# Optimization experiments

Hardware: AMD Instinct MI355X
Metric: run time of the kernel (lower is better)

Reference implementation:

```python
import jax, jax.numpy as jnp
import numpy as np

G, NP, F = 128, 1024, 16   # graphs, nodes per graph, node feature dim
K = 16                      # kNN neighbors (includes self, as in PyG knn)
H, L, OUT = 64, 64, 128     # edge-MLP hidden, latent, final output dims


def setup_inputs() -> dict:
    key = jax.random.key(0)
    ks = jax.random.split(key, 5)
    def w(i, shape, fan):
        return jax.random.normal(ks[i], shape, jnp.float32) / np.sqrt(fan)
    return {
        "x": jax.random.normal(ks[0], (G * NP, F), jnp.float32),
        "batch": jnp.repeat(jnp.arange(G, dtype=jnp.int32), NP),  # equal-size graphs
        "W1": w(1, (2 * F, H), 2 * F), "b1": jnp.zeros((H,), jnp.float32),
        "W2": w(2, (H, L), H),         "b2": jnp.zeros((L,), jnp.float32),
        "Wf": w(3, (L, OUT), L),       "bf": jnp.zeros((OUT,), jnp.float32),
    }


def reference(x, batch, W1, b1, W2, b2, Wf, bf):
    # batch = repeat(arange(G), NP) -> equal-size graphs, reshape instead of segment ops
    xg = x.reshape(G, NP, F)
    # dynamic kNN within each graph (squared euclidean, self included like PyG knn)
    sq = jnp.sum(xg * xg, axis=-1)                                   # [G,NP]
    dist = sq[:, :, None] + sq[:, None, :] - 2.0 * jnp.einsum('gif,gjf->gij', xg, xg)
    _, idx = jax.lax.top_k(-dist, K)                                 # [G,NP,K]
    # gather neighbor features x_j
    xj = jnp.take_along_axis(xg[:, None, :, :], idx[..., None], axis=2)  # [G,NP,K,F]
    xi = xg[:, :, None, :]                                           # [G,NP,1,F]
    e = jnp.concatenate([jnp.broadcast_to(xi, xj.shape), xj - xi], axis=-1)  # [G,NP,K,2F]
    # edge MLP [2F -> H -> L], ReLU between, plain last layer
    h = jax.nn.relu(e @ W1 + b1)
    h = h @ W2 + b2                                                  # [G,NP,K,L]
    node = jnp.mean(h, axis=2)                                       # mean aggregation  [G,NP,L]
    g = jnp.mean(node, axis=1)                                       # global_mean_pool  [G,L]
    return g @ Wf + bf                                               # final linear     [G,OUT]
```

## Files before the change

### kernel.cpp

```cpp
#include <hip/hip_runtime.h>
#include <hip/hip_bf16.h>
#include <stdint.h>

#define G_    128
#define NP_   1024
#define F_    16
#define K_    16
#define H_    64
#define L_    64
#define OUT_  128

typedef short  short8v  __attribute__((ext_vector_type(8)));
typedef float  f32x16   __attribute__((ext_vector_type(16)));
typedef float  f32x4    __attribute__((ext_vector_type(4)));

__device__ __forceinline__ uint16_t bf_rne(float f) {
    uint32_t u = __float_as_uint(f);
    return (uint16_t)((u + 0x7FFFu + ((u >> 16) & 1u)) >> 16);
}
__device__ __forceinline__ float bf_to_f(uint16_t h) {
    return __uint_as_float((uint32_t)h << 16);
}

__global__ __launch_bounds__(512, 4) void knn_kernel(
    const float* __restrict__ x, int* __restrict__ idxw)
{
    __shared__ uint16_t zh[2048 * 8];
    __shared__ uint16_t zl[2048 * 8];
    __shared__ float    sqarr[32 * 2 * 16];

    const int b   = blockIdx.x;
    const int g   = b >> 2;
    const float* xg = x + (size_t)g * NP_ * F_;
    const int tid  = threadIdx.x;
    const int lane = tid & 63;
    const int wave = tid >> 6;
    const int hi   = lane >> 5;
    const int col  = lane & 31;

#pragma unroll
    for (int rr = 0; rr < 2; ++rr) {
        const int row = tid * 2 + rr;
        const float4* xr = (const float4*)(xg + (size_t)row * 16);
        float4 c0 = xr[0], c1 = xr[1], c2 = xr[2], c3 = xr[3];
        float fv[16] = {c0.x,c0.y,c0.z,c0.w, c1.x,c1.y,c1.z,c1.w,
                        c2.x,c2.y,c2.z,c2.w, c3.x,c3.y,c3.z,c3.w};
        float sq = 0.f;
#pragma unroll
        for (int e = 0; e < 16; ++e) sq = fmaf(fv[e], fv[e], sq);

        short8v hv0, hv1, lv0, lv1;
#pragma unroll
        for (int e = 0; e < 8; ++e) {
            uint16_t hb = bf_rne(fv[e]);
            hv0[e] = (short)hb;
            lv0[e] = (short)bf_rne(fv[e] - bf_to_f(hb));
        }
#pragma unroll
        for (int e = 0; e < 8; ++e) {
            uint16_t hb = bf_rne(fv[8 + e]);
            hv1[e] = (short)hb;
            lv1[e] = (short)bf_rne(fv[8 + e] - bf_to_f(hb));
        }
        const int e0 = ((row >> 5) << 6) + (row & 31);
        *(short8v*)&zh[(size_t)e0 * 8]        = hv0;
        *(short8v*)&zh[(size_t)(e0 + 32) * 8] = hv1;
        *(short8v*)&zl[(size_t)e0 * 8]        = lv0;
        *(short8v*)&zl[(size_t)(e0 + 32) * 8] = lv1;
        const int s2 = ((row >> 5) << 1) + ((row >> 2) & 1);
        const int r  = (row & 3) | (((row >> 3) & 3) << 2);
        sqarr[s2 * 16 + r] = sq;
    }

    const int qbase = (b & 3) * 256 + wave * 32;
    short8v Bh, Bl;
    {
        const float* qsrc = xg + (size_t)(qbase + col) * 16 + hi * 8;
        float4 q0 = ((const float4*)qsrc)[0];
        float4 q1 = ((const float4*)qsrc)[1];
        float qv[8] = {q0.x,q0.y,q0.z,q0.w, q1.x,q1.y,q1.z,q1.w};
#pragma unroll
        for (int e = 0; e < 8; ++e) {
            float m2 = -2.f * qv[e];
            uint16_t hb = bf_rne(m2);
            Bh[e] = (short)hb;
            Bl[e] = (short)bf_rne(m2 - bf_to_f(hb));
        }
    }

    float hp[16];
#pragma unroll
    for (int m = 0; m < 16; ++m) hp[m] = __uint_as_float(0x7F000000u);

    __syncthreads();

    const int hi4 = hi << 2;

#define CE(a, i, j) { float t_lo = fminf(a[i], a[j]);                         \
                      float t_hi = fmaxf(a[i], a[j]);                         \
                      a[i] = t_lo; a[j] = t_hi; }

#pragma unroll 2
    for (int s = 0; s < 32; ++s) {
        short8v Ah = *(const short8v*)&zh[(size_t)(s * 64 + lane) * 8];
        short8v Al = *(const short8v*)&zl[(size_t)(s * 64 + lane) * 8];
        const float* sqb = &sqarr[(s * 2 + hi) * 16];
        f32x4 q0 = *(const f32x4*)(sqb + 0);
        f32x4 q1 = *(const f32x4*)(sqb + 4);
        f32x4 q2 = *(const f32x4*)(sqb + 8);
        f32x4 q3 = *(const f32x4*)(sqb + 12);

        f32x16 acc = {q0[0],q0[1],q0[2],q0[3], q1[0],q1[1],q1[2],q1[3],
                      q2[0],q2[1],q2[2],q2[3], q3[0],q3[1],q3[2],q3[3]};
        acc = __builtin_amdgcn_mfma_f32_32x32x16_bf16(Ah, Bl, acc, 0, 0, 0);
        acc = __builtin_amdgcn_mfma_f32_32x32x16_bf16(Al, Bh, acc, 0, 0, 0);
        acc = __builtin_amdgcn_mfma_f32_32x32x16_bf16(Ah, Bh, acc, 0, 0, 0);

        const uint32_t jb = ((uint32_t)s << 5) | (uint32_t)hi4;
        float kk[16];
#pragma unroll
        for (int r = 0; r < 16; ++r) {
            uint32_t jv = jb | (uint32_t)((r & 3) + 8 * (r >> 2));
            kk[r] = __uint_as_float((__float_as_uint(acc[r]) & 0xFFFFFC00u) | jv);
        }

        CE(kk,0,1)  CE(kk,2,3)  CE(kk,4,5)  CE(kk,6,7)
        CE(kk,8,9)  CE(kk,10,11) CE(kk,12,13) CE(kk,14,15)
        CE(kk,0,2)  CE(kk,1,3)  CE(kk,4,6)  CE(kk,5,7)
        CE(kk,8,10) CE(kk,9,11) CE(kk,12,14) CE(kk,13,15)
        CE(kk,1,2)  CE(kk,5,6)  CE(kk,9,10) CE(kk,13,14)
        CE(kk,0,4)  CE(kk,1,5)  CE(kk,2,6)  CE(kk,3,7)
        CE(kk,8,12) CE(kk,9,13) CE(kk,10,14) CE(kk,11,15)
        CE(kk,2,4)  CE(kk,3,5)  CE(kk,10,12) CE(kk,11,13)
        CE(kk,1,2)  CE(kk,3,4)  CE(kk,5,6)
        CE(kk,9,10) CE(kk,11,12) CE(kk,13,14)
        CE(kk,0,8)  CE(kk,1,9)  CE(kk,2,10) CE(kk,3,11)
        CE(kk,4,12) CE(kk,5,13) CE(kk,6,14) CE(kk,7,15)
        CE(kk,4,8)  CE(kk,5,9)  CE(kk,6,10) CE(kk,7,11)
        CE(kk,2,4)  CE(kk,3,5)  CE(kk,6,8)  CE(kk,7,9)
        CE(kk,10,12) CE(kk,11,13)
        CE(kk,1,2)  CE(kk,3,4)  CE(kk,5,6)  CE(kk,7,8)
        CE(kk,9,10) CE(kk,11,12) CE(kk,13,14)

        float c[16];
#pragma unroll
        for (int i = 0; i < 16; ++i) c[i] = fminf(hp[i], kk[15 - i]);
        CE(c,0,8)  CE(c,1,9)  CE(c,2,10) CE(c,3,11)
        CE(c,4,12) CE(c,5,13) CE(c,6,14) CE(c,7,15)
        CE(c,0,4)  CE(c,1,5)  CE(c,2,6)  CE(c,3,7)
        CE(c,8,12) CE(c,9,13) CE(c,10,14) CE(c,11,15)
        CE(c,0,2)  CE(c,1,3)  CE(c,4,6)  CE(c,5,7)
        CE(c,8,10) CE(c,9,11) CE(c,12,14) CE(c,13,15)
        CE(c,0,1)  CE(c,2,3)  CE(c,4,5)  CE(c,6,7)
        CE(c,8,9)  CE(c,10,11) CE(c,12,13) CE(c,14,15)
#pragma unroll
        for (int i = 0; i < 16; ++i) hp[i] = c[i];
    }
#undef CE

    float ot[16];
#pragma unroll
    for (int m = 0; m < 16; ++m) ot[m] = __shfl_xor(hp[m], 32);
#pragma unroll
    for (int m = 0; m < 16; ++m) {
        float kf = ot[m];
#pragma unroll
        for (int t = 15; t >= 1; --t)
            hp[t] = __builtin_amdgcn_fmed3f(kf, hp[t - 1], hp[t]);
        hp[0] = fminf(hp[0], kf);
    }

    if (lane < 32) {
        int* row = idxw + ((size_t)g * NP_ + qbase + col) * K_;
#pragma unroll
        for (int m4 = 0; m4 < 4; ++m4) {
            int4 o;
            o.x = (int)(__float_as_uint(hp[m4 * 4 + 0]) & 1023u);
            o.y = (int)(__float_as_uint(hp[m4 * 4 + 1]) & 1023u);
            o.z = (int)(__float_as_uint(hp[m4 * 4 + 2]) & 1023u);
            o.w = (int)(__float_as_uint(hp[m4 * 4 + 3]) & 1023u);
            *(int4*)(row + m4 * 4) = o;
        }
    }
}

__global__ __launch_bounds__(256) void v_kernel(
    const float* __restrict__ x, const float* __restrict__ W1,
    float* __restrict__ v)
{
    const int lane = threadIdx.x & 63;
    const int wave = threadIdx.x >> 6;

    float wb[16];
#pragma unroll
    for (int f = 0; f < 16; ++f) wb[f] = W1[(16 + f) * 64 + lane];

    const int base = blockIdx.x * 64 + wave * 16;
    for (int n = 0; n < 16; ++n) {
        const int p = base + n;
        const float4* xr = (const float4*)(x + (size_t)p * 16);
        float4 a0 = xr[0], a1 = xr[1], a2 = xr[2], a3 = xr[3];
        float xv[16] = {a0.x,a0.y,a0.z,a0.w, a1.x,a1.y,a1.z,a1.w,
                        a2.x,a2.y,a2.z,a2.w, a3.x,a3.y,a3.z,a3.w};
        float vv = 0.f;
#pragma unroll
        for (int f = 0; f < 16; ++f) vv = fmaf(xv[f], wb[f], vv);
        v[(size_t)p * 64 + lane] = vv;
    }
}

__global__ __launch_bounds__(256) void gather_kernel(
    const float* __restrict__ x, const float* __restrict__ W1,
    const float* __restrict__ b1, const float* __restrict__ v,
    const int* __restrict__ idxw, float* __restrict__ P)
{
    const int lane = threadIdx.x & 63;
    const int wave = threadIdx.x >> 6;
    const int b    = blockIdx.x;
    const int xcd  = b & 7, slot = b >> 3;
    const int g    = xcd + ((slot & 15) << 3);
    const int chunk = slot >> 4;
    const int pbase = g * NP_ + chunk * 128 + wave * 32;

    float wd[16];
#pragma unroll
    for (int f = 0; f < 16; ++f)
        wd[f] = W1[f * 64 + lane] - W1[(16 + f) * 64 + lane];
    const float bias = b1[lane];

    const float* vg = v + ((size_t)g << 16);
    float acc = 0.f;
    for (int n = 0; n < 32; ++n) {
        const int ii = pbase + n;
        const float4* xr = (const float4*)(x + (size_t)ii * 16);
        float4 c0 = xr[0], c1 = xr[1], c2 = xr[2], c3 = xr[3];
        float uu = bias;
        uu = fmaf(c0.x, wd[0],  uu); uu = fmaf(c0.y, wd[1],  uu);
        uu = fmaf(c0.z, wd[2],  uu); uu = fmaf(c0.w, wd[3],  uu);
        uu = fmaf(c1.x, wd[4],  uu); uu = fmaf(c1.y, wd[5],  uu);
        uu = fmaf(c1.z, wd[6],  uu); uu = fmaf(c1.w, wd[7],  uu);
        uu = fmaf(c2.x, wd[8],  uu); uu = fmaf(c2.y, wd[9],  uu);
        uu = fmaf(c2.z, wd[10], uu); uu = fmaf(c2.w, wd[11], uu);
        uu = fmaf(c3.x, wd[12], uu); uu = fmaf(c3.y, wd[13], uu);
        uu = fmaf(c3.z, wd[14], uu); uu = fmaf(c3.w, wd[15], uu);

        const int4* irow = (const int4*)(idxw + (size_t)ii * 16);
#pragma unroll
        for (int q = 0; q < 4; ++q) {
            int4 j4 = irow[q];
            float v0 = vg[((size_t)j4.x << 6) + lane];
            float v1 = vg[((size_t)j4.y << 6) + lane];
            float v2 = vg[((size_t)j4.z << 6) + lane];
            float v3 = vg[((size_t)j4.w << 6) + lane];
            acc += fmaxf(0.f, uu + v0);
            acc += fmaxf(0.f, uu + v1);
            acc += fmaxf(0.f, uu + v2);
            acc += fmaxf(0.f, uu + v3);
        }
    }
    P[(size_t)(((g << 3) + chunk) * 4 + wave) * 64 + lane] = acc;
}

__global__ __launch_bounds__(128) void head_kernel(
    const float* __restrict__ P, const float* __restrict__ W2,
    const float* __restrict__ b2, const float* __restrict__ Wf,
    const float* __restrict__ bf, float* __restrict__ out)
{
    __shared__ float hbar[64];
    __shared__ float t[64];
    const int g = blockIdx.x;
    const int tid = threadIdx.x;
    if (tid < 64) {
        float s = 0.f;
        const float* pr = P + (size_t)g * 32 * 64 + tid;
#pragma unroll
        for (int i = 0; i < 32; ++i) s += pr[i * 64];
        hbar[tid] = s * (1.f / (1024.f * 16.f));
    }
    __syncthreads();
    if (tid < 64) {
        float a = b2[tid];
        for (int h = 0; h < 64; ++h) a = fmaf(hbar[h], W2[h * 64 + tid], a);
        t[tid] = a;
    }
    __syncthreads();
    float a = bf[tid];
    for (int h = 0; h < 64; ++h) a = fmaf(t[h], Wf[h * 128 + tid], a);
    out[g * 128 + tid] = a;
}

extern "C" void kernel_launch(void* const* d_in, const int* in_sizes, int n_in,
                              void* d_out, int out_size, void* d_ws, size_t ws_size,
                              hipStream_t stream)
{
    const float* x  = (const float*)d_in[0];
    const float* W1 = (const float*)d_in[2];
    const float* b1 = (const float*)d_in[3];
    const float* W2 = (const float*)d_in[4];
    const float* b2 = (const float*)d_in[5];
    const float* Wf = (const float*)d_in[6];
    const float* bf = (const float*)d_in[7];
    float* out = (float*)d_out;

    char* ws = (char*)d_ws;
    const size_t MB = 1024 * 1024;
    float* v    = (float*)ws;
    int*   idxw = (int*)(ws + 32 * MB);
    float* P    = (float*)(ws + 40 * MB);

    knn_kernel   <<<G_ * 4, 512, 0, stream>>>(x, idxw);
    v_kernel     <<<2048, 256, 0, stream>>>(x, W1, v);
    gather_kernel<<<G_ * 8, 256, 0, stream>>>(x, W1, b1, v, idxw, P);
    head_kernel  <<<G_, 128, 0, stream>>>(P, W2, b2, Wf, bf, out);
}
```

Before: 148.5 us.

## Split kNN prep into separate kernel and split candidate range across waves

Moves the bf16 hi/lo split and squared-norm computation into a separate prep kernel that writes to global workspace, so the kNN kernel reads candidates straight from global/L2 instead of rebuilding them in LDS in every block. The kNN grid doubles to 1024 blocks. Each block now handles 128 queries, and the two halves of the candidate range go to different waves whose top-16 lists are merged through a small shared buffer with a bitonic merge. Blocks are also remapped so that blocks of the same graph land on the same XCD. This trades redundant per-block prep and the large LDS footprint for an extra launch, global traffic, and a shared-memory merge step.

```diff
diff --git a/kernel.cpp b/kernel.cpp
--- a/kernel.cpp
+++ b/kernel.cpp
@@ -22,60 +22,66 @@
     return __uint_as_float((uint32_t)h << 16);
 }
 
-__global__ __launch_bounds__(512, 4) void knn_kernel(
-    const float* __restrict__ x, int* __restrict__ idxw)
-{
-    __shared__ uint16_t zh[2048 * 8];
-    __shared__ uint16_t zl[2048 * 8];
-    __shared__ float    sqarr[32 * 2 * 16];
-
-    const int b   = blockIdx.x;
-    const int g   = b >> 2;
-    const float* xg = x + (size_t)g * NP_ * F_;
+__global__ __launch_bounds__(256) void prep_kernel(
+    const float* __restrict__ x, uint16_t* __restrict__ zh,
+    uint16_t* __restrict__ zl, float* __restrict__ sqp)
+{
+    const int p = blockIdx.x * 256 + threadIdx.x;
+    const float4* xr = (const float4*)(x + (size_t)p * 16);
+    float4 c0 = xr[0], c1 = xr[1], c2 = xr[2], c3 = xr[3];
+    float fv[16] = {c0.x,c0.y,c0.z,c0.w, c1.x,c1.y,c1.z,c1.w,
+                    c2.x,c2.y,c2.z,c2.w, c3.x,c3.y,c3.z,c3.w};
+    float sq = 0.f;
+#pragma unroll
+    for (int e = 0; e < 16; ++e) sq = fmaf(fv[e], fv[e], sq);
+
+    short8v hv0, hv1, lv0, lv1;
+#pragma unroll
+    for (int e = 0; e < 8; ++e) {
+        uint16_t hb = bf_rne(fv[e]);
+        hv0[e] = (short)hb;
+        lv0[e] = (short)bf_rne(fv[e] - bf_to_f(hb));
+    }
+#pragma unroll
+    for (int e = 0; e < 8; ++e) {
+        uint16_t hb = bf_rne(fv[8 + e]);
+        hv1[e] = (short)hb;
+        lv1[e] = (short)bf_rne(fv[8 + e] - bf_to_f(hb));
+    }
+    const size_t eb = (size_t)(p >> 5) * 64 + (p & 31);
+    *(short8v*)&zh[eb * 8]        = hv0;
+    *(short8v*)&zh[(eb + 32) * 8] = hv1;
+    *(short8v*)&zl[eb * 8]        = lv0;
+    *(short8v*)&zl[(eb + 32) * 8] = lv1;
+
+    const int r32 = p & 31;
+    const int hi  = (r32 >> 2) & 1;
+    const int r   = (r32 & 3) | ((r32 >> 3) << 2);
+    sqp[(size_t)((p >> 5) << 5) + (hi << 4) + r] = sq;
+}
+
+__global__ __launch_bounds__(512, 8) void knn_kernel(
+    const float* __restrict__ x, const uint16_t* __restrict__ zh,
+    const uint16_t* __restrict__ zl, const float* __restrict__ sqp,
+    int* __restrict__ idxw)
+{
+    __shared__ float mrg[4][32][17];
+
+    const int b    = blockIdx.x;
+    const int xcd  = b & 7, slot = b >> 3;
+    const int g    = xcd + ((slot & 15) << 3);
+    const int qoct = slot >> 4;
     const int tid  = threadIdx.x;
     const int lane = tid & 63;
-    const int wave = tid >> 6;
+    const int w    = tid >> 6;
+    const int qtile = w & 3, jh = w >> 2;
+    const int col  = lane & 31;
     const int hi   = lane >> 5;
-    const int col  = lane & 31;
-
-#pragma unroll
-    for (int rr = 0; rr < 2; ++rr) {
-        const int row = tid * 2 + rr;
-        const float4* xr = (const float4*)(xg + (size_t)row * 16);
-        float4 c0 = xr[0], c1 = xr[1], c2 = xr[2], c3 = xr[3];
-        float fv[16] = {c0.x,c0.y,c0.z,c0.w, c1.x,c1.y,c1.z,c1.w,
-                        c2.x,c2.y,c2.z,c2.w, c3.x,c3.y,c3.z,c3.w};
-        float sq = 0.f;
-#pragma unroll
-        for (int e = 0; e < 16; ++e) sq = fmaf(fv[e], fv[e], sq);
-
-        short8v hv0, hv1, lv0, lv1;
-#pragma unroll
-        for (int e = 0; e < 8; ++e) {
-            uint16_t hb = bf_rne(fv[e]);
-            hv0[e] = (short)hb;
-            lv0[e] = (short)bf_rne(fv[e] - bf_to_f(hb));
-        }
-#pragma unroll
-        for (int e = 0; e < 8; ++e) {
-            uint16_t hb = bf_rne(fv[8 + e]);
-            hv1[e] = (short)hb;
-            lv1[e] = (short)bf_rne(fv[8 + e] - bf_to_f(hb));
-        }
-        const int e0 = ((row >> 5) << 6) + (row & 31);
-        *(short8v*)&zh[(size_t)e0 * 8]        = hv0;
-        *(short8v*)&zh[(size_t)(e0 + 32) * 8] = hv1;
-        *(short8v*)&zl[(size_t)e0 * 8]        = lv0;
-        *(short8v*)&zl[(size_t)(e0 + 32) * 8] = lv1;
-        const int s2 = ((row >> 5) << 1) + ((row >> 2) & 1);
-        const int r  = (row & 3) | (((row >> 3) & 3) << 2);
-        sqarr[s2 * 16 + r] = sq;
-    }
-
-    const int qbase = (b & 3) * 256 + wave * 32;
+    const int qbase = qoct * 128 + qtile * 32;
+
     short8v Bh, Bl;
     {
-        const float* qsrc = xg + (size_t)(qbase + col) * 16 + hi * 8;
+        const float* qsrc = x + ((size_t)g * NP_ + qbase + col) * 16 + hi * 8;
         float4 q0 = ((const float4*)qsrc)[0];
         float4 q1 = ((const float4*)qsrc)[1];
         float qv[8] = {q0.x,q0.y,q0.z,q0.w, q1.x,q1.y,q1.z,q1.w};
@@ -88,27 +94,45 @@
         }
     }
 
+    const uint16_t* zhg = zh + (size_t)(g * 32) * 64 * 8;
+    const uint16_t* zlg = zl + (size_t)(g * 32) * 64 * 8;
+    const float*    sqg = sqp + ((size_t)g << 10) + (hi << 4);
+    const uint32_t  hib = (uint32_t)(hi << 2);
+
     float hp[16];
 #pragma unroll
     for (int m = 0; m < 16; ++m) hp[m] = __uint_as_float(0x7F000000u);
-
-    __syncthreads();
-
-    const int hi4 = hi << 2;
 
 #define CE(a, i, j) { float t_lo = fminf(a[i], a[j]);                         \
                       float t_hi = fmaxf(a[i], a[j]);                         \
                       a[i] = t_lo; a[j] = t_hi; }
+#define BMERGE(hp, ol)                                                        \
+    {                                                                         \
+        float c[16];                                                          \
+        _Pragma("unroll")                                                     \
+        for (int i = 0; i < 16; ++i) c[i] = fminf(hp[i], ol[15 - i]);         \
+        CE(c,0,8)  CE(c,1,9)  CE(c,2,10) CE(c,3,11)                           \
+        CE(c,4,12) CE(c,5,13) CE(c,6,14) CE(c,7,15)                           \
+        CE(c,0,4)  CE(c,1,5)  CE(c,2,6)  CE(c,3,7)                            \
+        CE(c,8,12) CE(c,9,13) CE(c,10,14) CE(c,11,15)                         \
+        CE(c,0,2)  CE(c,1,3)  CE(c,4,6)  CE(c,5,7)                            \
+        CE(c,8,10) CE(c,9,11) CE(c,12,14) CE(c,13,15)                         \
+        CE(c,0,1)  CE(c,2,3)  CE(c,4,5)  CE(c,6,7)                            \
+        CE(c,8,9)  CE(c,10,11) CE(c,12,13) CE(c,14,15)                        \
+        _Pragma("unroll")                                                     \
+        for (int i = 0; i < 16; ++i) hp[i] = c[i];                            \
+    }
 
 #pragma unroll 2
-    for (int s = 0; s < 32; ++s) {
-        short8v Ah = *(const short8v*)&zh[(size_t)(s * 64 + lane) * 8];
-        short8v Al = *(const short8v*)&zl[(size_t)(s * 64 + lane) * 8];
-        const float* sqb = &sqarr[(s * 2 + hi) * 16];
-        f32x4 q0 = *(const f32x4*)(sqb + 0);
-        f32x4 q1 = *(const f32x4*)(sqb + 4);
-        f32x4 q2 = *(const f32x4*)(sqb + 8);
-        f32x4 q3 = *(const f32x4*)(sqb + 12);
+    for (int si = 0; si < 16; ++si) {
+        const int s = (jh << 4) + si;
+        short8v Ah = *(const short8v*)&zhg[(size_t)(s * 64 + lane) * 8];
+        short8v Al = *(const short8v*)&zlg[(size_t)(s * 64 + lane) * 8];
+        const float* sb = sqg + s * 32;
+        f32x4 q0 = *(const f32x4*)(sb + 0);
+        f32x4 q1 = *(const f32x4*)(sb + 4);
+        f32x4 q2 = *(const f32x4*)(sb + 8);
+        f32x4 q3 = *(const f32x4*)(sb + 12);
 
         f32x16 acc = {q0[0],q0[1],q0[2],q0[3], q1[0],q1[1],q1[2],q1[3],
                       q2[0],q2[1],q2[2],q2[3], q3[0],q3[1],q3[2],q3[3]};
@@ -116,7 +140,7 @@
         acc = __builtin_amdgcn_mfma_f32_32x32x16_bf16(Al, Bh, acc, 0, 0, 0);
         acc = __builtin_amdgcn_mfma_f32_32x32x16_bf16(Ah, Bh, acc, 0, 0, 0);
 
-        const uint32_t jb = ((uint32_t)s << 5) | (uint32_t)hi4;
+        const uint32_t jb = ((uint32_t)s << 5) | hib;
         float kk[16];
 #pragma unroll
         for (int r = 0; r < 16; ++r) {
@@ -142,35 +166,27 @@
         CE(kk,1,2)  CE(kk,3,4)  CE(kk,5,6)  CE(kk,7,8)
         CE(kk,9,10) CE(kk,11,12) CE(kk,13,14)
 
-        float c[16];
-#pragma unroll
-        for (int i = 0; i < 16; ++i) c[i] = fminf(hp[i], kk[15 - i]);
-        CE(c,0,8)  CE(c,1,9)  CE(c,2,10) CE(c,3,11)
-        CE(c,4,12) CE(c,5,13) CE(c,6,14) CE(c,7,15)
-        CE(c,0,4)  CE(c,1,5)  CE(c,2,6)  CE(c,3,7)
-        CE(c,8,12) CE(c,9,13) CE(c,10,14) CE(c,11,15)
-        CE(c,0,2)  CE(c,1,3)  CE(c,4,6)  CE(c,5,7)
-        CE(c,8,10) CE(c,9,11) CE(c,12,14) CE(c,13,15)
-        CE(c,0,1)  CE(c,2,3)  CE(c,4,5)  CE(c,6,7)
-        CE(c,8,9)  CE(c,10,11) CE(c,12,13) CE(c,14,15)
-#pragma unroll
-        for (int i = 0; i < 16; ++i) hp[i] = c[i];
-    }
-#undef CE
-
-    float ot[16];
-#pragma unroll
-    for (int m = 0; m < 16; ++m) ot[m] = __shfl_xor(hp[m], 32);
-#pragma unroll
-    for (int m = 0; m < 16; ++m) {
-        float kf = ot[m];
-#pragma unroll
-        for (int t = 15; t >= 1; --t)
-            hp[t] = __builtin_amdgcn_fmed3f(kf, hp[t - 1], hp[t]);
-        hp[0] = fminf(hp[0], kf);
-    }
-
-    if (lane < 32) {
+        BMERGE(hp, kk)
+    }
+
+    {
+        float ot[16];
+#pragma unroll
+        for (int m = 0; m < 16; ++m) ot[m] = __shfl_xor(hp[m], 32);
+        BMERGE(hp, ot)
+    }
+
+    if (jh == 1 && lane < 32) {
+#pragma unroll
+        for (int m = 0; m < 16; ++m) mrg[qtile][col][m] = hp[m];
+    }
+    __syncthreads();
+    if (jh == 0 && lane < 32) {
+        float ot[16];
+#pragma unroll
+        for (int m = 0; m < 16; ++m) ot[m] = mrg[qtile][col][m];
+        BMERGE(hp, ot)
+
         int* row = idxw + ((size_t)g * NP_ + qbase + col) * K_;
 #pragma unroll
         for (int m4 = 0; m4 < 4; ++m4) {
@@ -182,6 +198,8 @@
             *(int4*)(row + m4 * 4) = o;
         }
     }
+#undef BMERGE
+#undef CE
 }
 
 __global__ __launch_bounds__(256) void v_kernel(
@@ -303,12 +321,17 @@
     float* out = (float*)d_out;
 
     char* ws = (char*)d_ws;
+    const size_t N  = (size_t)G_ * NP_;
     const size_t MB = 1024 * 1024;
-    float* v    = (float*)ws;
-    int*   idxw = (int*)(ws + 32 * MB);
-    float* P    = (float*)(ws + 40 * MB);
-
-    knn_kernel   <<<G_ * 4, 512, 0, stream>>>(x, idxw);
+    float*    v    = (float*)ws;
+    int*      idxw = (int*)(ws + 32 * MB);
+    float*    P    = (float*)(ws + 40 * MB);
+    uint16_t* zh   = (uint16_t*)(ws + 41 * MB);
+    uint16_t* zl   = (uint16_t*)(ws + 45 * MB);
+    float*    sqp  = (float*)(ws + 49 * MB);
+
+    prep_kernel  <<<(int)(N / 256), 256, 0, stream>>>(x, zh, zl, sqp);
+    knn_kernel   <<<G_ * 8, 512, 0, stream>>>(x, zh, zl, sqp, idxw);
     v_kernel     <<<2048, 256, 0, stream>>>(x, W1, v);
     gather_kernel<<<G_ * 8, 256, 0, stream>>>(x, W1, b1, v, idxw, P);
     head_kernel  <<<G_, 128, 0, stream>>>(P, W2, b2, Wf, bf, out);
```

Result: slower. 155.3 us (+4.6%).
